# Kernel tuning notes

Hardware: AMD Instinct MI355X
Metric: run time of the kernel (lower is better)

The kernel has to match this reference:

```python
import jax, jax.numpy as jnp
import numpy as np
import math

D_MODEL = 256
N_HEAD = 8
D_FF = 1024
WINDOW = 3
RADIUS = 4
NEG = -1e9


def rmsnorm(x, g):
    eps = jnp.asarray(jnp.finfo(x.dtype).eps, x.dtype)
    return x * jax.lax.rsqrt(jnp.mean(x * x, axis=-1, keepdims=True) + eps) * g


def mha(x, Wqkv, bqkv, Wo, bo, mask):
    # x: [B, S, D]; mask: [S, S] bool, True = disallowed
    B, S, D = x.shape
    hd = D // N_HEAD
    qkv = x @ Wqkv.T + bqkv
    q, k, v = jnp.split(qkv, 3, axis=-1)
    q = q.reshape(B, S, N_HEAD, hd).transpose(0, 2, 1, 3)
    k = k.reshape(B, S, N_HEAD, hd).transpose(0, 2, 1, 3)
    v = v.reshape(B, S, N_HEAD, hd).transpose(0, 2, 1, 3)
    scores = jnp.einsum('bhqd,bhkd->bhqk', q, k) / math.sqrt(hd)
    scores = jnp.where(mask[None, None], jnp.asarray(NEG, scores.dtype), scores)
    attn = jax.nn.softmax(scores, axis=-1)
    o = jnp.einsum('bhqk,bhkd->bhqd', attn, v)
    o = o.transpose(0, 2, 1, 3).reshape(B, S, D)
    return o @ Wo.T + bo


def setup_inputs() -> dict:
    key = jax.random.key(0)
    ks = jax.random.split(key, 16)
    d, dff = D_MODEL, D_FF
    sc = 0.02
    inp = {
        'x': jax.random.normal(ks[0], (4, 16384, d), dtype=jnp.float32),
        'coords': jax.random.randint(ks[1], (128, 2), 0, 12),
        'spatial_size': 128,
        'Wqkv_s': jax.random.normal(ks[2], (3 * d, d), jnp.float32) * sc,
        'bqkv_s': jnp.zeros((3 * d,), jnp.float32),
        'Wo_s': jax.random.normal(ks[3], (d, d), jnp.float32) * sc,
        'bo_s': jnp.zeros((d,), jnp.float32),
        'Wqkv_t': jax.random.normal(ks[4], (3 * d, d), jnp.float32) * sc,
        'bqkv_t': jnp.zeros((3 * d,), jnp.float32),
        'Wo_t': jax.random.normal(ks[5], (d, d), jnp.float32) * sc,
        'bo_t': jnp.zeros((d,), jnp.float32),
        'g1': jnp.ones((d,), jnp.float32),
        'g2': jnp.ones((d,), jnp.float32),
        'g3': jnp.ones((d,), jnp.float32),
        'W1': jax.random.normal(ks[6], (dff, d), jnp.float32) * sc,
        'b1': jnp.zeros((dff,), jnp.float32),
        'W2': jax.random.normal(ks[7], (d, dff), jnp.float32) * sc,
        'b2': jnp.zeros((d,), jnp.float32),
    }
    return inp


def reference(x, coords, spatial_size, Wqkv_s, bqkv_s, Wo_s, bo_s,
              Wqkv_t, bqkv_t, Wo_t, bo_t, g1, g2, g3, W1, b1, W2, b2):
    b, seq, d = x.shape
    s = int(spatial_size)
    t = seq // s

    # spatial mask: Chebyshev distance between 2D coords > RADIUS -> masked
    dx = jnp.abs(coords[:, 0][:, None] - coords[:, 0][None, :])
    dy = jnp.abs(coords[:, 1][:, None] - coords[:, 1][None, :])
    smask = jnp.maximum(dx, dy) > RADIUS  # [s, s]

    # temporal mask: attend only to keys j with 0 <= i - j <= WINDOW
    idx = jnp.arange(t)
    dd = idx[:, None] - idx[None, :]
    tmask = ~((dd >= 0) & (dd <= WINDOW))  # [t, t]

    x4 = x.reshape(b, t, s, d)

    # spatial attention over s within each (b, t)
    xs = x4.reshape(b * t, s, d)
    y_s = mha(rmsnorm(xs, g1), Wqkv_s, bqkv_s, Wo_s, bo_s, smask)
    x4 = x4 + y_s.reshape(b, t, s, d)

    # temporal attention over t within each (b, s)
    x_t = x4.transpose(0, 2, 1, 3).reshape(b * s, t, d)
    y_t = mha(rmsnorm(x_t, g2), Wqkv_t, bqkv_t, Wo_t, bo_t, tmask)
    x4 = x4 + y_t.reshape(b, s, t, d).transpose(0, 2, 1, 3)

    # FFN (exact GELU, matching torch nn.GELU default)
    h = rmsnorm(x4, g3)
    y = jax.nn.gelu(h @ W1.T + b1, approximate=False) @ W2.T + b2
    x4 = x4 + y
    return x4.reshape(b, seq, d)
```

## Files before the change

kernel.cpp:

```cpp
#include <hip/hip_runtime.h>
#include <hip/hip_bf16.h>

typedef __attribute__((ext_vector_type(4))) float f32x4;
typedef __attribute__((ext_vector_type(8))) short bf16x8;
typedef __attribute__((ext_vector_type(4))) unsigned short u16x4;

#define NTOK 65536
#define DMODEL 256
#define DFF 1024
#define NH 8
#define HD 32
#define SSP 128
#define TLEN 128
#define SCALE 0.17677669529663687f

__device__ __forceinline__ float bf2f(unsigned short u) {
    return __builtin_bit_cast(float, (unsigned int)u << 16);
}
__device__ __forceinline__ unsigned short f2bf(float f) {
    unsigned int u = __builtin_bit_cast(unsigned int, f);
    unsigned int r = u + 0x7fffu + ((u >> 16) & 1u);
    return (unsigned short)(r >> 16);
}
__device__ __forceinline__ void gload_lds16(const void* g, void* l) {
    __builtin_amdgcn_global_load_lds((const __attribute__((address_space(1))) void*)g,
                                     (__attribute__((address_space(3))) void*)l, 16, 0, 0);
}

__global__ __launch_bounds__(256)
void cvt_w(const float* __restrict__ a, const float* __restrict__ b,
           const float* __restrict__ c, const float* __restrict__ d,
           const float* __restrict__ e, const float* __restrict__ f,
           unsigned short* __restrict__ o)
{
    int i = blockIdx.x * 256 + threadIdx.x;
    float v;
    if      (i < 196608)  v = a[i];
    else if (i < 262144)  v = b[i - 196608];
    else if (i < 458752)  v = c[i - 262144];
    else if (i < 524288)  v = d[i - 458752];
    else if (i < 786432)  v = e[i - 524288];
    else                  v = f[i - 786432];
    o[i] = f2bf(v);
}

__global__ __launch_bounds__(256)
void rms_copy(const float* __restrict__ x, const float* __restrict__ g,
              float* __restrict__ xo, unsigned short* __restrict__ xn)
{
    const int row = blockIdx.x * 4 + (threadIdx.x >> 6);
    const int lane = threadIdx.x & 63;
    const float4 v = *(const float4*)&x[(size_t)row * DMODEL + lane * 4];
    float s = v.x * v.x + v.y * v.y + v.z * v.z + v.w * v.w;
    #pragma unroll
    for (int o = 1; o < 64; o <<= 1) s += __shfl_xor(s, o);
    const float rinv = rsqrtf(s * (1.0f / DMODEL) + 1.1920929e-7f);
    *(float4*)&xo[(size_t)row * DMODEL + lane * 4] = v;
    const float4 gv = *(const float4*)&g[lane * 4];
    u16x4 o4;
    o4[0] = f2bf(v.x * rinv * gv.x);
    o4[1] = f2bf(v.y * rinv * gv.y);
    o4[2] = f2bf(v.z * rinv * gv.z);
    o4[3] = f2bf(v.w * rinv * gv.w);
    *(u16x4*)&xn[(size_t)row * DMODEL + lane * 4] = o4;
}

template<int EPI>
__global__ __launch_bounds__(256)
void gemm_bt(const unsigned short* __restrict__ A,
             const unsigned short* __restrict__ W,
             const float* __restrict__ bias,
             unsigned short* __restrict__ Cb,
             float* __restrict__ Cf,
             int N, int K, int NCT)
{
    __shared__ unsigned short lds[17408];
    unsigned short* As = lds;
    unsigned short* Bs = lds + 8192;

    const int tid = threadIdx.x;
    const int wave = tid >> 6, lane = tid & 63;
    const int wr = wave >> 1, wc = wave & 1;

    const int nwg = gridDim.x;
    const int bid = blockIdx.x;
    const int lin = (bid & 7) * (nwg >> 3) + (bid >> 3);
    const int row0 = (lin / NCT) * 128;
    const int col0 = (lin % NCT) * 128;

    f32x4 acc[4][4];
    #pragma unroll
    for (int i = 0; i < 4; i++)
        #pragma unroll
        for (int j = 0; j < 4; j++)
            acc[i][j] = (f32x4){0.f, 0.f, 0.f, 0.f};

    const int srow  = tid >> 3;
    const int kx    = ((tid & 7) * 8) ^ ((srow & 7) * 8);

    const int fr = lane & 15, g = lane >> 4;
    const int sw = (fr & 7) * 8;

    for (int k0 = 0; k0 < K; k0 += 64) {
        #pragma unroll
        for (int q = 0; q < 4; q++) {
            const int row = q * 32 + srow;
            gload_lds16(A + (size_t)(row0 + row) * K + k0 + kx, As + q * 2048 + tid * 8);
            gload_lds16(W + (size_t)(col0 + row) * K + k0 + kx, Bs + q * 2048 + tid * 8);
        }
        __syncthreads();
        #pragma unroll
        for (int kh = 0; kh < 2; kh++) {
            const int ke = (kh * 32 + g * 8) ^ sw;
            bf16x8 af[4], bw[4];
            #pragma unroll
            for (int i = 0; i < 4; i++)
                af[i] = *(const bf16x8*)&As[(wr * 64 + i * 16 + fr) * 64 + ke];
            #pragma unroll
            for (int j = 0; j < 4; j++)
                bw[j] = *(const bf16x8*)&Bs[(wc * 64 + j * 16 + fr) * 64 + ke];
            #pragma unroll
            for (int i = 0; i < 4; i++)
                #pragma unroll
                for (int j = 0; j < 4; j++)
                    acc[i][j] = __builtin_amdgcn_mfma_f32_16x16x32_bf16(af[i], bw[j], acc[i][j], 0, 0, 0);
        }
        __syncthreads();
    }

    if constexpr (EPI == 2) {
        #pragma unroll
        for (int i = 0; i < 4; i++) {
            #pragma unroll
            for (int j = 0; j < 4; j++) {
                const int col = col0 + wc * 64 + j * 16 + fr;
                const float bv = bias[col];
                #pragma unroll
                for (int r = 0; r < 4; r++) {
                    const int row = row0 + wr * 64 + i * 16 + g * 4 + r;
                    Cf[(size_t)row * N + col] += acc[i][j][r] + bv;
                }
            }
        }
    } else {
        #pragma unroll
        for (int i = 0; i < 4; i++) {
            #pragma unroll
            for (int j = 0; j < 4; j++) {
                const int col = wc * 64 + j * 16 + fr;
                const float bv = bias[col0 + col];
                #pragma unroll
                for (int r = 0; r < 4; r++) {
                    float v = acc[i][j][r] + bv;
                    if constexpr (EPI == 1) {
                        const float y = 1.5957691216057308f * (v + 0.044715f * v * v * v);
                        v = v / (1.0f + __expf(-y));
                    }
                    lds[(wr * 64 + i * 16 + g * 4 + r) * 136 + col] = f2bf(v);
                }
            }
        }
        __syncthreads();
        #pragma unroll
        for (int q = 0; q < 8; q++) {
            const int chunk = q * 256 + tid;
            const int row = chunk >> 4, c16 = chunk & 15;
            *(bf16x8*)&Cb[(size_t)(row0 + row) * N + col0 + c16 * 8] =
                *(const bf16x8*)&lds[row * 136 + c16 * 8];
        }
    }
}

__global__ __launch_bounds__(256)
void gemm_rms(const unsigned short* __restrict__ A,
              const unsigned short* __restrict__ W,
              const float* __restrict__ bias,
              float* __restrict__ xo,
              const float* __restrict__ gv,
              unsigned short* __restrict__ xn,
              int K)
{
    __shared__ unsigned short As[64 * 64];
    __shared__ unsigned short Bs[256 * 64];
    __shared__ float red[64 * 4];

    const int tid = threadIdx.x;
    const int wave = tid >> 6, lane = tid & 63;
    const int fr = lane & 15, g4 = lane >> 4;

    const int nwg = gridDim.x;
    const int bid = blockIdx.x;
    const int lin = (bid & 7) * (nwg >> 3) + (bid >> 3);
    const int row0 = lin * 64;

    f32x4 acc[4][4];
    #pragma unroll
    for (int i = 0; i < 4; i++)
        #pragma unroll
        for (int j = 0; j < 4; j++)
            acc[i][j] = (f32x4){0.f, 0.f, 0.f, 0.f};

    const int srow = tid >> 3;
    const int kx   = ((tid & 7) * 8) ^ ((srow & 7) * 8);
    const int sw   = (fr & 7) * 8;

    for (int k0 = 0; k0 < K; k0 += 64) {
        #pragma unroll
        for (int p = 0; p < 2; p++)
            gload_lds16(A + (size_t)(row0 + p * 32 + srow) * K + k0 + kx, As + p * 2048 + tid * 8);
        #pragma unroll
        for (int p = 0; p < 8; p++)
            gload_lds16(W + (size_t)(p * 32 + srow) * K + k0 + kx, Bs + p * 2048 + tid * 8);
        __syncthreads();
        #pragma unroll
        for (int kh = 0; kh < 2; kh++) {
            const int ke = (kh * 32 + g4 * 8) ^ sw;
            bf16x8 af[4], bw[4];
            #pragma unroll
            for (int i = 0; i < 4; i++)
                af[i] = *(const bf16x8*)&As[(i * 16 + fr) * 64 + ke];
            #pragma unroll
            for (int j = 0; j < 4; j++)
                bw[j] = *(const bf16x8*)&Bs[(wave * 64 + j * 16 + fr) * 64 + ke];
            #pragma unroll
            for (int i = 0; i < 4; i++)
                #pragma unroll
                for (int j = 0; j < 4; j++)
                    acc[i][j] = __builtin_amdgcn_mfma_f32_16x16x32_bf16(af[i], bw[j], acc[i][j], 0, 0, 0);
        }
        __syncthreads();
    }

    #pragma unroll
    for (int i = 0; i < 4; i++) {
        #pragma unroll
        for (int j = 0; j < 4; j++) {
            const int col = wave * 64 + j * 16 + fr;
            const float bv = bias[col];
            #pragma unroll
            for (int r = 0; r < 4; r++) {
                const int row = row0 + i * 16 + g4 * 4 + r;
                const float xv = xo[(size_t)row * DMODEL + col] + acc[i][j][r] + bv;
                xo[(size_t)row * DMODEL + col] = xv;
                acc[i][j][r] = xv;
            }
        }
    }
    #pragma unroll
    for (int i = 0; i < 4; i++) {
        #pragma unroll
        for (int r = 0; r < 4; r++) {
            float p = acc[i][0][r] * acc[i][0][r] + acc[i][1][r] * acc[i][1][r]
                    + acc[i][2][r] * acc[i][2][r] + acc[i][3][r] * acc[i][3][r];
            #pragma unroll
            for (int o = 1; o < 16; o <<= 1) p += __shfl_xor(p, o);
            if (fr == 0) red[(i * 16 + g4 * 4 + r) * 4 + wave] = p;
        }
    }
    __syncthreads();
    #pragma unroll
    for (int i = 0; i < 4; i++) {
        #pragma unroll
        for (int r = 0; r < 4; r++) {
            const int rl = i * 16 + g4 * 4 + r;
            const float rsq = red[rl * 4 + 0] + red[rl * 4 + 1] + red[rl * 4 + 2] + red[rl * 4 + 3];
            const float rinv = rsqrtf(rsq * (1.0f / DMODEL) + 1.1920929e-7f);
            #pragma unroll
            for (int j = 0; j < 4; j++) {
                const int col = wave * 64 + j * 16 + fr;
                xn[(size_t)(row0 + rl) * DMODEL + col] = f2bf(acc[i][j][r] * rinv * gv[col]);
            }
        }
    }
}

__global__ __launch_bounds__(256)
void attn_spatial(const unsigned short* __restrict__ qkv,
                  const int* __restrict__ coords,
                  unsigned short* __restrict__ out)
{
    __shared__ unsigned short Qs[128 * 32];
    __shared__ unsigned short Ks[128 * 32];
    __shared__ unsigned short Vt[32 * 136];
    __shared__ unsigned short Pb[64 * 132];
    __shared__ int cx[128], cy[128];

    const int bt = blockIdx.x, h = blockIdx.y;
    const int tid = threadIdx.x, wave = tid >> 6, lane = tid & 63;
    const size_t base = (size_t)bt * SSP * 768 + (size_t)h * HD;

    {
        const int rr = tid >> 1, cb = (tid & 1) * 16;
        const unsigned short* p = qkv + base + (size_t)rr * 768 + cb;
        *(bf16x8*)&Qs[rr * 32 + cb]     = *(const bf16x8*)p;
        *(bf16x8*)&Qs[rr * 32 + cb + 8] = *(const bf16x8*)(p + 8);
        p += 256;
        *(bf16x8*)&Ks[rr * 32 + cb]     = *(const bf16x8*)p;
        *(bf16x8*)&Ks[rr * 32 + cb + 8] = *(const bf16x8*)(p + 8);
        p += 256;
        bf16x8 v0 = *(const bf16x8*)p, v1 = *(const bf16x8*)(p + 8);
        #pragma unroll
        for (int e = 0; e < 8; e++) {
            Vt[(cb + e) * 136 + rr]     = (unsigned short)v0[e];
            Vt[(cb + 8 + e) * 136 + rr] = (unsigned short)v1[e];
        }
        if (tid < 128) { cx[tid] = coords[2 * tid]; cy[tid] = coords[2 * tid + 1]; }
    }
    __syncthreads();

    const int fr = lane & 15;
    const int g  = lane >> 4;
    const int fko = g * 8;

    for (int half = 0; half < 2; half++) {
        const int rbase = half * 64 + wave * 16;
        bf16x8 aq = *(const bf16x8*)&Qs[(rbase + fr) * 32 + fko];
        f32x4 sc[8];
        #pragma unroll
        for (int tj = 0; tj < 8; tj++) {
            bf16x8 bk = *(const bf16x8*)&Ks[(tj * 16 + fr) * 32 + fko];
            sc[tj] = __builtin_amdgcn_mfma_f32_16x16x32_bf16(aq, bk, (f32x4){0.f,0.f,0.f,0.f}, 0, 0, 0);
        }
        int cxi[4], cyi[4];
        #pragma unroll
        for (int r = 0; r < 4; r++) { const int i = rbase + g * 4 + r; cxi[r] = cx[i]; cyi[r] = cy[i]; }
        float m[4] = {-1e30f, -1e30f, -1e30f, -1e30f};
        #pragma unroll
        for (int tj = 0; tj < 8; tj++) {
            const int j = tj * 16 + fr;
            const int cxj = cx[j], cyj = cy[j];
            #pragma unroll
            for (int r = 0; r < 4; r++) {
                int dx = cxi[r] - cxj; dx = dx < 0 ? -dx : dx;
                int dy = cyi[r] - cyj; dy = dy < 0 ? -dy : dy;
                const float v = ((dx > dy ? dx : dy) > 4) ? -1e9f : sc[tj][r] * SCALE;
                sc[tj][r] = v;
                m[r] = fmaxf(m[r], v);
            }
        }
        #pragma unroll
        for (int r = 0; r < 4; r++) {
            #pragma unroll
            for (int o = 1; o < 16; o <<= 1) m[r] = fmaxf(m[r], __shfl_xor(m[r], o));
        }
        float sm[4] = {0.f, 0.f, 0.f, 0.f};
        #pragma unroll
        for (int tj = 0; tj < 8; tj++) {
            #pragma unroll
            for (int r = 0; r < 4; r++) {
                const float e = __expf(sc[tj][r] - m[r]);
                sc[tj][r] = e;
                sm[r] += e;
            }
        }
        #pragma unroll
        for (int r = 0; r < 4; r++) {
            #pragma unroll
            for (int o = 1; o < 16; o <<= 1) sm[r] += __shfl_xor(sm[r], o);
        }
        float inv[4];
        #pragma unroll
        for (int r = 0; r < 4; r++) inv[r] = 1.0f / sm[r];
        #pragma unroll
        for (int tj = 0; tj < 8; tj++) {
            #pragma unroll
            for (int r = 0; r < 4; r++)
                Pb[(wave * 16 + g * 4 + r) * 132 + tj * 16 + fr] = f2bf(sc[tj][r] * inv[r]);
        }
        #pragma unroll
        for (int td = 0; td < 2; td++) {
            f32x4 o = (f32x4){0.f, 0.f, 0.f, 0.f};
            #pragma unroll
            for (int kk = 0; kk < 4; kk++) {
                bf16x8 pa = *(const bf16x8*)&Pb[(wave * 16 + fr) * 132 + kk * 32 + fko];
                bf16x8 bv = *(const bf16x8*)&Vt[(td * 16 + fr) * 136 + kk * 32 + fko];
                o = __builtin_amdgcn_mfma_f32_16x16x32_bf16(pa, bv, o, 0, 0, 0);
            }
            #pragma unroll
            for (int r = 0; r < 4; r++) {
                const int i = half * 64 + wave * 16 + g * 4 + r;
                const int d = td * 16 + fr;
                out[((size_t)(bt * SSP + i)) * DMODEL + h * HD + d] = f2bf(o[r]);
            }
        }
    }
}

__device__ __forceinline__ float dot32(const float* __restrict__ qr,
                                       const unsigned short* __restrict__ Kt, int j)
{
    float a = 0.f;
    #pragma unroll
    for (int d = 0; d < 32; d++) a += qr[d] * bf2f(Kt[d * 128 + j]);
    return a;
}

__global__ __launch_bounds__(128)
void attn_temporal(const unsigned short* __restrict__ qkv,
                   unsigned short* __restrict__ out)
{
    __shared__ unsigned short Kt[32 * 128], Vt[32 * 128];
    const int bs = blockIdx.x, h = blockIdx.y;
    const int b = bs >> 7, sp = bs & 127;
    const int tid = threadIdx.x;
    const size_t rb = ((size_t)b * 16384 + (size_t)tid * 128 + sp) * 768 + (size_t)h * HD;
    bf16x8 qreg[4];
    #pragma unroll
    for (int c = 0; c < 4; c++) {
        qreg[c] = *(const bf16x8*)(qkv + rb + c * 8);
        bf16x8 k = *(const bf16x8*)(qkv + rb + 256 + c * 8);
        bf16x8 v = *(const bf16x8*)(qkv + rb + 512 + c * 8);
        #pragma unroll
        for (int e = 0; e < 8; e++) {
            const int d = c * 8 + e;
            Kt[d * 128 + tid] = (unsigned short)k[e];
            Vt[d * 128 + tid] = (unsigned short)v[e];
        }
    }
    __syncthreads();

    const int i = tid;
    float qr[32];
    #pragma unroll
    for (int d = 0; d < 32; d++) qr[d] = bf2f((unsigned short)qreg[d >> 3][d & 7]);

    float s0 = -1e30f, s1 = -1e30f, s2 = -1e30f;
    if (i >= 3) s0 = dot32(qr, Kt, i - 3) * SCALE;
    if (i >= 2) s1 = dot32(qr, Kt, i - 2) * SCALE;
    if (i >= 1) s2 = dot32(qr, Kt, i - 1) * SCALE;
    const float s3 = dot32(qr, Kt, i) * SCALE;

    const float mx = fmaxf(fmaxf(s0, s1), fmaxf(s2, s3));
    const float p0 = __expf(s0 - mx), p1 = __expf(s1 - mx), p2 = __expf(s2 - mx), p3 = __expf(s3 - mx);
    const float inv = 1.0f / (p0 + p1 + p2 + p3);
    const int j0 = i >= 3 ? i - 3 : 0;
    const int j1 = i >= 2 ? i - 2 : 0;
    const int j2 = i >= 1 ? i - 1 : 0;
    const size_t ob = ((size_t)b * 16384 + (size_t)i * 128 + sp) * DMODEL + (size_t)h * HD;
    #pragma unroll
    for (int d = 0; d < 32; d++) {
        const float o = (p0 * bf2f(Vt[d * 128 + j0]) + p1 * bf2f(Vt[d * 128 + j1]) +
                         p2 * bf2f(Vt[d * 128 + j2]) + p3 * bf2f(Vt[d * 128 + i])) * inv;
        out[ob + d] = f2bf(o);
    }
}

extern "C" void kernel_launch(void* const* d_in, const int* in_sizes, int n_in,
                              void* d_out, int out_size, void* d_ws, size_t ws_size,
                              hipStream_t stream)
{
    const float* x_in   = (const float*)d_in[0];
    const int*   coords = (const int*)d_in[1];
    const float* Wqkv_s = (const float*)d_in[3];
    const float* bqkv_s = (const float*)d_in[4];
    const float* Wo_s   = (const float*)d_in[5];
    const float* bo_s   = (const float*)d_in[6];
    const float* Wqkv_t = (const float*)d_in[7];
    const float* bqkv_t = (const float*)d_in[8];
    const float* Wo_t   = (const float*)d_in[9];
    const float* bo_t   = (const float*)d_in[10];
    const float* g1     = (const float*)d_in[11];
    const float* g2     = (const float*)d_in[12];
    const float* g3     = (const float*)d_in[13];
    const float* W1     = (const float*)d_in[14];
    const float* b1     = (const float*)d_in[15];
    const float* W2     = (const float*)d_in[16];
    const float* b2     = (const float*)d_in[17];
    float* xo = (float*)d_out;

    char* ws = (char*)d_ws;
    unsigned short* wb  = (unsigned short*)ws;
    unsigned short* xn  = (unsigned short*)(ws + (size_t)2 * 1024 * 1024);
    unsigned short* big = (unsigned short*)(ws + (size_t)34 * 1024 * 1024);

    unsigned short* wQKVs = wb;
    unsigned short* wOs   = wb + 196608;
    unsigned short* wQKVt = wb + 262144;
    unsigned short* wOt   = wb + 458752;
    unsigned short* w1b   = wb + 524288;
    unsigned short* w2b   = wb + 786432;

    cvt_w<<<4096, 256, 0, stream>>>(Wqkv_s, Wo_s, Wqkv_t, Wo_t, W1, W2, wb);

    rms_copy<<<16384, 256, 0, stream>>>(x_in, g1, xo, xn);
    gemm_bt<0><<<3072, 256, 0, stream>>>(xn, wQKVs, bqkv_s, big, nullptr, 768, 256, 6);
    attn_spatial<<<dim3(512, 8), 256, 0, stream>>>(big, coords, xn);
    gemm_rms<<<1024, 256, 0, stream>>>(xn, wOs, bo_s, xo, g2, xn, 256);

    gemm_bt<0><<<3072, 256, 0, stream>>>(xn, wQKVt, bqkv_t, big, nullptr, 768, 256, 6);
    attn_temporal<<<dim3(512, 8), 128, 0, stream>>>(big, xn);
    gemm_rms<<<1024, 256, 0, stream>>>(xn, wOt, bo_t, xo, g3, xn, 256);

    gemm_bt<1><<<4096, 256, 0, stream>>>(xn, w1b, b1, big, nullptr, 1024, 256, 8);
    gemm_bt<2><<<1024, 256, 0, stream>>>(big, w2b, b2, nullptr, xo, 256, 1024, 2);
}
```

Before: 641.1 us.

## Fuse FFN up-projection, GELU and down-projection into one kernel

Measured after the change: 559.6 us. -12.7%, faster.

```diff
diff --git a/kernel.cpp b/kernel.cpp
--- a/kernel.cpp
+++ b/kernel.cpp
@@ -152,10 +152,6 @@
                 #pragma unroll
                 for (int r = 0; r < 4; r++) {
                     float v = acc[i][j][r] + bv;
-                    if constexpr (EPI == 1) {
-                        const float y = 1.5957691216057308f * (v + 0.044715f * v * v * v);
-                        v = v / (1.0f + __expf(-y));
-                    }
                     lds[(wr * 64 + i * 16 + g * 4 + r) * 136 + col] = f2bf(v);
                 }
             }
@@ -269,6 +265,133 @@
             for (int j = 0; j < 4; j++) {
                 const int col = wave * 64 + j * 16 + fr;
                 xn[(size_t)(row0 + rl) * DMODEL + col] = f2bf(acc[i][j][r] * rinv * gv[col]);
+            }
+        }
+    }
+}
+
+__global__ __launch_bounds__(256)
+void ffn_fused(const unsigned short* __restrict__ A,
+               const unsigned short* __restrict__ W1,
+               const float* __restrict__ b1,
+               const unsigned short* __restrict__ W2,
+               const float* __restrict__ b2,
+               float* __restrict__ xo)
+{
+    __shared__ unsigned short As[64 * 64];
+    __shared__ unsigned short Bs[256 * 64];
+    __shared__ unsigned short Hs[64 * 264];
+
+    const int tid = threadIdx.x;
+    const int wave = tid >> 6, lane = tid & 63;
+    const int fr = lane & 15, g = lane >> 4;
+
+    const int nwg = gridDim.x;
+    const int bid = blockIdx.x;
+    const int lin = (bid & 7) * (nwg >> 3) + (bid >> 3);
+    const int row0 = lin * 64;
+
+    const int srow = tid >> 3;
+    const int kx   = ((tid & 7) * 8) ^ ((srow & 7) * 8);
+    const int sw   = (fr & 7) * 8;
+
+    f32x4 acc2[4][4];
+    #pragma unroll
+    for (int i = 0; i < 4; i++)
+        #pragma unroll
+        for (int j = 0; j < 4; j++)
+            acc2[i][j] = (f32x4){0.f, 0.f, 0.f, 0.f};
+
+    for (int c = 0; c < 4; c++) {
+        f32x4 accH[4][4];
+        #pragma unroll
+        for (int i = 0; i < 4; i++)
+            #pragma unroll
+            for (int j = 0; j < 4; j++)
+                accH[i][j] = (f32x4){0.f, 0.f, 0.f, 0.f};
+
+        for (int k0 = 0; k0 < 256; k0 += 64) {
+            #pragma unroll
+            for (int p = 0; p < 2; p++)
+                gload_lds16(A + (size_t)(row0 + p * 32 + srow) * DMODEL + k0 + kx,
+                            As + p * 2048 + tid * 8);
+            #pragma unroll
+            for (int p = 0; p < 8; p++)
+                gload_lds16(W1 + (size_t)(c * 256 + p * 32 + srow) * DMODEL + k0 + kx,
+                            Bs + p * 2048 + tid * 8);
+            __syncthreads();
+            #pragma unroll
+            for (int kh = 0; kh < 2; kh++) {
+                const int ke = (kh * 32 + g * 8) ^ sw;
+                bf16x8 af[4], bw[4];
+                #pragma unroll
+                for (int i = 0; i < 4; i++)
+                    af[i] = *(const bf16x8*)&As[(i * 16 + fr) * 64 + ke];
+                #pragma unroll
+                for (int j = 0; j < 4; j++)
+                    bw[j] = *(const bf16x8*)&Bs[(wave * 64 + j * 16 + fr) * 64 + ke];
+                #pragma unroll
+                for (int i = 0; i < 4; i++)
+                    #pragma unroll
+                    for (int j = 0; j < 4; j++)
+                        accH[i][j] = __builtin_amdgcn_mfma_f32_16x16x32_bf16(af[i], bw[j], accH[i][j], 0, 0, 0);
+            }
+            __syncthreads();
+        }
+
+        #pragma unroll
+        for (int j = 0; j < 4; j++) {
+            const int col = wave * 64 + j * 16 + fr;
+            const float bv = b1[c * 256 + col];
+            #pragma unroll
+            for (int i = 0; i < 4; i++) {
+                #pragma unroll
+                for (int r = 0; r < 4; r++) {
+                    float v = accH[i][j][r] + bv;
+                    v = 0.5f * v * (1.0f + erff(v * 0.70710678118654752f));
+                    Hs[(i * 16 + g * 4 + r) * 264 + col] = f2bf(v);
+                }
+            }
+        }
+        __syncthreads();
+
+        for (int k0 = 0; k0 < 256; k0 += 64) {
+            #pragma unroll
+            for (int p = 0; p < 8; p++)
+                gload_lds16(W2 + (size_t)(p * 32 + srow) * DFF + c * 256 + k0 + kx,
+                            Bs + p * 2048 + tid * 8);
+            __syncthreads();
+            #pragma unroll
+            for (int kh = 0; kh < 2; kh++) {
+                const int keh = k0 + kh * 32 + g * 8;
+                const int ke  = (kh * 32 + g * 8) ^ sw;
+                bf16x8 ha[4], bw[4];
+                #pragma unroll
+                for (int i = 0; i < 4; i++)
+                    ha[i] = *(const bf16x8*)&Hs[(i * 16 + fr) * 264 + keh];
+                #pragma unroll
+                for (int j = 0; j < 4; j++)
+                    bw[j] = *(const bf16x8*)&Bs[(wave * 64 + j * 16 + fr) * 64 + ke];
+                #pragma unroll
+                for (int i = 0; i < 4; i++)
+                    #pragma unroll
+                    for (int j = 0; j < 4; j++)
+                        acc2[i][j] = __builtin_amdgcn_mfma_f32_16x16x32_bf16(ha[i], bw[j], acc2[i][j], 0, 0, 0);
+            }
+            __syncthreads();
+        }
+    }
+
+    #pragma unroll
+    for (int j = 0; j < 4; j++) {
+        const int col = wave * 64 + j * 16 + fr;
+        const float bv = b2[col];
+        #pragma unroll
+        for (int i = 0; i < 4; i++) {
+            #pragma unroll
+            for (int r = 0; r < 4; r++) {
+                const int row = row0 + i * 16 + g * 4 + r;
+                xo[(size_t)row * DMODEL + col] += acc2[i][j][r] + bv;
             }
         }
     }
@@ -491,6 +614,5 @@
     attn_temporal<<<dim3(512, 8), 128, 0, stream>>>(big, xn);
     gemm_rms<<<1024, 256, 0, stream>>>(xn, wOt, bo_t, xo, g3, xn, 256);
 
-    gemm_bt<1><<<4096, 256, 0, stream>>>(xn, w1b, b1, big, nullptr, 1024, 256, 8);
-    gemm_bt<2><<<1024, 256, 0, stream>>>(big, w2b, b2, nullptr, xo, 256, 1024, 2);
-}
+    ffn_fused<<<1024, 256, 0, stream>>>(xn, w1b, b1, w2b, b2, xo);
+}
```

## Fuse FFN up-projection, GELU and down-projection into one kernel

Applied to the files above, without the earlier changes.

Measured after the change: 859.3 us. 1.34x slower.

```diff
diff --git a/kernel.cpp b/kernel.cpp
--- a/kernel.cpp
+++ b/kernel.cpp
@@ -152,10 +152,6 @@
                 #pragma unroll
                 for (int r = 0; r < 4; r++) {
                     float v = acc[i][j][r] + bv;
-                    if constexpr (EPI == 1) {
-                        const float y = 1.5957691216057308f * (v + 0.044715f * v * v * v);
-                        v = v / (1.0f + __expf(-y));
-                    }
                     lds[(wr * 64 + i * 16 + g * 4 + r) * 136 + col] = f2bf(v);
                 }
             }
@@ -269,6 +265,115 @@
             for (int j = 0; j < 4; j++) {
                 const int col = wave * 64 + j * 16 + fr;
                 xn[(size_t)(row0 + rl) * DMODEL + col] = f2bf(acc[i][j][r] * rinv * gv[col]);
+            }
+        }
+    }
+}
+
+__global__ __launch_bounds__(256, 3)
+void ffn_fused(const unsigned short* __restrict__ A,
+               const unsigned short* __restrict__ W1,
+               const float* __restrict__ b1,
+               const unsigned short* __restrict__ W2,
+               const float* __restrict__ b2,
+               float* __restrict__ xo)
+{
+    __shared__ unsigned short Bs[2][128 * 64];
+    __shared__ unsigned short Hs[4][16 * 136];
+
+    const int tid = threadIdx.x;
+    const int wave = tid >> 6, lane = tid & 63;
+    const int fr = lane & 15, g = lane >> 4;
+
+    const int nwg = gridDim.x, bid = blockIdx.x;
+    const int lin = (bid & 7) * (nwg >> 3) + (bid >> 3);
+    const int row0 = lin * 64;
+
+    const int srow = tid >> 3;
+    const int kx   = ((tid & 7) * 8) ^ ((srow & 7) * 8);
+    const int sw   = (fr & 7) * 8;
+
+    f32x4 acc2[16];
+    #pragma unroll
+    for (int j = 0; j < 16; j++) acc2[j] = (f32x4){0.f, 0.f, 0.f, 0.f};
+    f32x4 acc1[8];
+
+    auto stage = [&](int b, int p) {
+        const int c = p >> 3, s = p & 7;
+        const unsigned short* src;
+        int rstride;
+        if (s < 4) { src = W1 + (size_t)(c * 128) * DMODEL + s * 64; rstride = DMODEL; }
+        else {
+            const int jg = (s - 4) >> 1, k0 = ((s - 4) & 1) * 64;
+            src = W2 + (size_t)(jg * 128) * DFF + c * 128 + k0; rstride = DFF;
+        }
+        #pragma unroll
+        for (int q = 0; q < 4; q++)
+            gload_lds16(src + (size_t)(q * 32 + srow) * rstride + kx,
+                        &Bs[b][q * 2048 + tid * 8]);
+    };
+
+    stage(0, 0);
+    __syncthreads();
+
+    for (int p = 0; p < 64; p++) {
+        const int b = p & 1, c = p >> 3, s = p & 7;
+        if (p + 1 < 64) stage(b ^ 1, p + 1);
+        if (s == 0) {
+            #pragma unroll
+            for (int j = 0; j < 8; j++) acc1[j] = (f32x4){0.f, 0.f, 0.f, 0.f};
+        }
+        if (s < 4) {
+            const int k0 = s * 64;
+            #pragma unroll
+            for (int kh = 0; kh < 2; kh++) {
+                const bf16x8 af = *(const bf16x8*)&A[(size_t)(row0 + wave * 16 + fr) * DMODEL
+                                                     + k0 + kh * 32 + g * 8];
+                const int ke = (kh * 32 + g * 8) ^ sw;
+                #pragma unroll
+                for (int j = 0; j < 8; j++) {
+                    const bf16x8 bw = *(const bf16x8*)&Bs[b][(j * 16 + fr) * 64 + ke];
+                    acc1[j] = __builtin_amdgcn_mfma_f32_16x16x32_bf16(af, bw, acc1[j], 0, 0, 0);
+                }
+            }
+        } else {
+            const int jg = (s - 4) >> 1, k0 = ((s - 4) & 1) * 64;
+            #pragma unroll
+            for (int kh = 0; kh < 2; kh++) {
+                const bf16x8 ha = *(const bf16x8*)&Hs[wave][fr * 136 + k0 + kh * 32 + g * 8];
+                const int ke = (kh * 32 + g * 8) ^ sw;
+                #pragma unroll
+                for (int j = 0; j < 8; j++) {
+                    const bf16x8 bw = *(const bf16x8*)&Bs[b][(j * 16 + fr) * 64 + ke];
+                    acc2[jg * 8 + j] = __builtin_amdgcn_mfma_f32_16x16x32_bf16(ha, bw, acc2[jg * 8 + j], 0, 0, 0);
+                }
+            }
+        }
+        if (s == 3) {
+            #pragma unroll
+            for (int j = 0; j < 8; j++) {
+                const float bv = b1[c * 128 + j * 16 + fr];
+                #pragma unroll
+                for (int r = 0; r < 4; r++) {
+                    float v = acc1[j][r] + bv;
+                    v = 0.5f * v * (1.0f + erff(v * 0.70710678118654752f));
+                    Hs[wave][(g * 4 + r) * 136 + j * 16 + fr] = f2bf(v);
+                }
+            }
+        }
+        __syncthreads();
+    }
+
+    #pragma unroll
+    for (int jg = 0; jg < 2; jg++) {
+        #pragma unroll
+        for (int j = 0; j < 8; j++) {
+            const int col = jg * 128 + j * 16 + fr;
+            const float bv = b2[col];
+            #pragma unroll
+            for (int r = 0; r < 4; r++) {
+                const int row = row0 + wave * 16 + g * 4 + r;
+                xo[(size_t)row * DMODEL + col] += acc2[jg * 8 + j][r] + bv;
             }
         }
     }
@@ -491,6 +596,5 @@
     attn_temporal<<<dim3(512, 8), 128, 0, stream>>>(big, xn);
     gemm_rms<<<1024, 256, 0, stream>>>(xn, wOt, bo_t, xo, g3, xn, 256);
 
-    gemm_bt<1><<<4096, 256, 0, stream>>>(xn, w1b, b1, big, nullptr, 1024, 256, 8);
-    gemm_bt<2><<<1024, 256, 0, stream>>>(big, w2b, b2, nullptr, xo, 256, 1024, 2);
-}
+    ffn_fused<<<1024, 256, 0, stream>>>(xn, w1b, b1, w2b, b2, xo);
+}
```
